# Kernel tuning notes

Hardware: AMD Instinct MI355X
Metric: run time of the kernel (lower is better)

The kernel has to match this reference:

```python
import jax, jax.numpy as jnp
import numpy as np

B, C, T = 32, 64, 4096
K = 256  # truncated memory length (kwargs['k'])


def setup_inputs() -> dict:
    key = jax.random.key(0)
    k1, k2 = jax.random.split(key)
    x = jax.random.normal(k1, (B, C, T), dtype=jnp.float32)
    epsilon = jax.random.normal(k2, (), dtype=jnp.float32)
    loc = jnp.asarray(0.5, dtype=jnp.float32)    # alpha_loc parameter
    scale = jnp.asarray(0.1, dtype=jnp.float32)  # alpha_scale parameter (pre-softplus)
    return {"x": x, "loc": loc, "scale": scale, "epsilon": epsilon, "k": K}


def _gl_coeffs(alpha, k, dtype):
    # Grunwald-Letnikov weights: w_0 = 1, w_j = w_{j-1} * (j - 1 - alpha) / j
    j = jnp.arange(k, dtype=dtype)
    factors = jnp.where(j == 0, jnp.asarray(1.0, dtype),
                        (j - 1.0 - alpha) / jnp.maximum(j, 1.0))
    return jnp.cumprod(factors)  # [k]


def reference(x, loc, scale, epsilon, k):
    # reparameterized fractional order (Normal prior): alpha = loc + softplus(scale) * eps
    alpha = loc + jax.nn.softplus(scale) * epsilon
    w = _gl_coeffs(alpha, k, x.dtype)  # [k]
    b, c, t = x.shape
    # truncated GL fractional derivative = causal depthwise conv with k taps:
    # out[n] = sum_{j=0}^{k-1} w_j * x[n-j]
    lhs = x.reshape(b * c, 1, t)                 # [N, 1, T]
    rhs = w[::-1].reshape(1, 1, k)               # [O=1, I=1, K] (flip for correlation)
    out = jax.lax.conv_general_dilated(lhs, rhs, window_strides=(1,),
                                       padding=[(k - 1, 0)])
    return out.reshape(b, c, t)
```

## Files before the change

kernel.cpp:

```cpp
#include <hip/hip_runtime.h>
#include <hip/hip_bf16.h>
#include <hip/hip_fp16.h>

#define TLEN 4096
#define KTAPS 256
#define NT 18
#define WCH 48

typedef __attribute__((ext_vector_type(8))) _Float16 f16x8;
typedef __attribute__((ext_vector_type(4))) unsigned int uint4v;
typedef __attribute__((ext_vector_type(16))) float f32x16;

static __device__ __forceinline__ unsigned int pkf16(float a, float b) {
    return __builtin_bit_cast(unsigned int, __builtin_amdgcn_cvt_pkrtz(a, b));
}

__global__ void __launch_bounds__(512, 4)
frac_conv_fused3(const float* __restrict__ x,
                 const float* __restrict__ loc,
                 const float* __restrict__ scale,
                 const float* __restrict__ eps,
                 float* __restrict__ out) {
    __shared__ unsigned int wrevp[320];
    __shared__ __align__(16) unsigned short Bf[WCH * 64 * 8];

    const int tid  = threadIdx.x;
    const int wave = tid >> 6;
    const int lane = tid & 63;
    const int l5   = lane >> 5;
    const int ln   = lane & 31;

    int rt, sg;
    {
        const int bid = blockIdx.x;
        if (gridDim.x == 512) {
            const int xcd = bid & 7;
            const int j   = bid >> 3;
            rt = xcd * 8 + (j & 7);
            sg = j >> 3;
        } else {
            rt = bid >> 3;
            sg = bid & 7;
        }
    }
    const int bn0 = sg * 512;

    const int r  = tid >> 4;
    const int cg = tid & 15;
    const float* __restrict__ xrow = x + (size_t)(rt * 32 + r) * TLEN;
    float4 v[12];
    #pragma unroll
    for (int jj = 0; jj < 12; ++jj) {
        const int w0 = cg * 4 + jj * 64;
        const int tg = bn0 - 256 + w0;
        v[jj] = (tg >= 0) ? *(const float4*)(xrow + tg) : make_float4(0.f, 0.f, 0.f, 0.f);
    }

    if (wave == 0) {
        const float alpha = loc[0] + log1pf(expf(scale[0])) * eps[0];
        const int j0 = 4 * lane;
        const float f0 = (j0 == 0) ? 1.0f : (((float)j0 - 1.0f - alpha) / (float)j0);
        const float f1 = (((float)j0 + 0.0f - alpha) / (float)(j0 + 1));
        const float f2 = (((float)j0 + 1.0f - alpha) / (float)(j0 + 2));
        const float f3 = (((float)j0 + 2.0f - alpha) / (float)(j0 + 3));
        const float p0 = f0, p1 = p0 * f1, p2 = p1 * f2, p3 = p2 * f3;
        float g = p3;
        #pragma unroll
        for (int dlt = 1; dlt < 64; dlt <<= 1) {
            const float t = __shfl_up(g, dlt, 64);
            if (lane >= dlt) g *= t;
        }
        float Sprev = __shfl_up(g, 1, 64);
        if (lane == 0) Sprev = 1.0f;
        const float q0 = Sprev * p0, q1 = Sprev * p1, q2 = Sprev * p2, q3 = g;
        const float wm1 = (lane == 0) ? 0.0f : Sprev;
        uint4v pk;
        pk[0] = pkf16(q3, q2);
        pk[1] = pkf16(q2, q1);
        pk[2] = pkf16(q1, q0);
        pk[3] = pkf16(q0, wm1);
        *(uint4v*)(wrevp + 284 - 4 * lane) = pk;
        if (lane == 63) wrevp[31] = pkf16(0.0f, q3);
        if (lane < 31)  wrevp[lane] = 0u;
        if (lane < 32)  wrevp[288 + lane] = 0u;
    }

    {
        uint2* Bf2 = (uint2*)Bf;
        #pragma unroll
        for (int jj = 0; jj < 12; ++jj) {
            const int w0 = cg * 4 + jj * 64;
            const int c  = w0 >> 4;
            const int h8 = (w0 >> 3) & 1;
            const int e0 = w0 & 7;
            const int uoff = (c * 64 + r + 32 * h8) * 8 + e0;
            Bf2[uoff >> 2] = make_uint2(pkf16(v[jj].x, v[jj].y),
                                        pkf16(v[jj].z, v[jj].w));
        }
    }
    __syncthreads();

    const int n0  = bn0 + wave * 64;
    const int lcb = wave * 4;
    const f16x8* Bv = (const f16x8*)Bf;
    const int o0 = 31 - ln + 8 * l5;

    auto LOADA = [&](int d) -> f16x8 {
        const int o = o0 + 16 * d;
        uint4v u;
        u[0] = wrevp[o];
        u[1] = wrevp[o + 2];
        u[2] = wrevp[o + 4];
        u[3] = wrevp[o + 6];
        return __builtin_bit_cast(f16x8, u);
    };

    f16x8 Afr[NT];
    f16x8 Bfr[NT + 2];
    Bfr[0] = Bv[(lcb + 0) * 64 + lane];
    Bfr[1] = Bv[(lcb + 1) * 64 + lane];
    Bfr[2] = Bv[(lcb + 2) * 64 + lane];
    Bfr[3] = Bv[(lcb + 3) * 64 + lane];
    Afr[0] = LOADA(0);
    Afr[1] = LOADA(1);

    f32x16 acc0 = {0.f, 0.f, 0.f, 0.f, 0.f, 0.f, 0.f, 0.f,
                   0.f, 0.f, 0.f, 0.f, 0.f, 0.f, 0.f, 0.f};
    f32x16 acc1 = acc0;

    #pragma unroll
    for (int d = 0; d < NT; ++d) {
        if (d + 4 < NT + 2) Bfr[d + 4] = Bv[(lcb + d + 4) * 64 + lane];
        if (d + 2 < NT)     Afr[d + 2] = LOADA(d + 2);
        acc0 = __builtin_amdgcn_mfma_f32_32x32x16_f16(Afr[d], Bfr[d],     acc0, 0, 0, 0);
        acc1 = __builtin_amdgcn_mfma_f32_32x32x16_f16(Afr[d], Bfr[d + 2], acc1, 0, 0, 0);
    }

    float* __restrict__ orow = out + (size_t)(rt * 32 + ln) * TLEN;
    #pragma unroll
    for (int g = 0; g < 4; ++g) {
        *(float4*)(orow + n0 + 8 * g + 4 * l5) =
            make_float4(acc0[4 * g + 0], acc0[4 * g + 1], acc0[4 * g + 2], acc0[4 * g + 3]);
        *(float4*)(orow + n0 + 32 + 8 * g + 4 * l5) =
            make_float4(acc1[4 * g + 0], acc1[4 * g + 1], acc1[4 * g + 2], acc1[4 * g + 3]);
    }
}

__global__ void gl_coeff_kernel(const float* __restrict__ loc,
                                const float* __restrict__ scale,
                                const float* __restrict__ eps,
                                float* __restrict__ w_out) {
    __shared__ float s[KTAPS];
    const int j = threadIdx.x;
    const float alpha = loc[0] + log1pf(expf(scale[0])) * eps[0];
    float f = (j == 0) ? 1.0f : (((float)j - 1.0f - alpha) / (float)j);
    s[j] = f;
    __syncthreads();
    #pragma unroll
    for (int st = 1; st < KTAPS; st <<= 1) {
        float v = s[j];
        float p = (j >= st) ? s[j - st] : 1.0f;
        __syncthreads();
        s[j] = v * p;
        __syncthreads();
    }
    w_out[j] = s[j];
}

__global__ void __launch_bounds__(256)
frac_conv_kernel(const float* __restrict__ x,
                 const float* __restrict__ w,
                 float* __restrict__ out) {
    __shared__ __align__(16) float xs[KTAPS + TLEN];
    __shared__ __align__(16) float wl[KTAPS];
    const int row = blockIdx.x;
    const int tid = threadIdx.x;
    const float* __restrict__ xr = x + (size_t)row * TLEN;
    float* __restrict__ orow = out + (size_t)row * TLEN;
    if (tid < 64) ((float4*)xs)[tid] = make_float4(0.f, 0.f, 0.f, 0.f);
    float4* xs4w = (float4*)(xs + KTAPS);
    const float4* xr4 = (const float4*)xr;
    #pragma unroll
    for (int k = 0; k < 4; ++k) xs4w[tid + k * 256] = xr4[tid + k * 256];
    if (tid < 64) ((float4*)wl)[tid] = ((const float4*)w)[tid];
    __syncthreads();
    const float4* __restrict__ xsv = (const float4*)xs;
    float4 acc[4]; float4 lo[4], hi[4]; int n0[4];
    #pragma unroll
    for (int g = 0; g < 4; ++g) {
        n0[g] = (tid << 2) + (g << 10);
        acc[g] = make_float4(0.f, 0.f, 0.f, 0.f);
        const int c = n0[g] >> 2;
        hi[g] = xsv[64 + c];
        lo[g] = xsv[63 + c];
    }
    #pragma unroll 4
    for (int j = 0; j < KTAPS - 4; j += 4) {
        const float4 w4 = *(const float4*)(wl + j);
        #pragma unroll
        for (int g = 0; g < 4; ++g) {
            acc[g].x += w4.x*hi[g].x + w4.y*lo[g].w + w4.z*lo[g].z + w4.w*lo[g].y;
            acc[g].y += w4.x*hi[g].y + w4.y*hi[g].x + w4.z*lo[g].w + w4.w*lo[g].z;
            acc[g].z += w4.x*hi[g].z + w4.y*hi[g].y + w4.z*hi[g].x + w4.w*lo[g].w;
            acc[g].w += w4.x*hi[g].w + w4.y*hi[g].z + w4.z*hi[g].y + w4.w*hi[g].x;
            hi[g] = lo[g];
            lo[g] = xsv[64 + ((n0[g] - j - 8) >> 2)];
        }
    }
    {
        const float4 w4 = *(const float4*)(wl + (KTAPS - 4));
        #pragma unroll
        for (int g = 0; g < 4; ++g) {
            acc[g].x += w4.x*hi[g].x + w4.y*lo[g].w + w4.z*lo[g].z + w4.w*lo[g].y;
            acc[g].y += w4.x*hi[g].y + w4.y*hi[g].x + w4.z*lo[g].w + w4.w*lo[g].z;
            acc[g].z += w4.x*hi[g].z + w4.y*hi[g].y + w4.z*hi[g].x + w4.w*lo[g].w;
            acc[g].w += w4.x*hi[g].w + w4.y*hi[g].z + w4.z*hi[g].y + w4.w*hi[g].x;
        }
    }
    #pragma unroll
    for (int g = 0; g < 4; ++g) *(float4*)(orow + n0[g]) = acc[g];
}

extern "C" void kernel_launch(void* const* d_in, const int* in_sizes, int n_in,
                              void* d_out, int out_size, void* d_ws, size_t ws_size,
                              hipStream_t stream) {
    const float* x     = (const float*)d_in[0];
    const float* loc   = (const float*)d_in[1];
    const float* scale = (const float*)d_in[2];
    const float* eps   = (const float*)d_in[3];
    float* out = (float*)d_out;
    const int rows = in_sizes[0] / TLEN;

    if ((rows % 32) == 0) {
        frac_conv_fused3<<<(rows / 32) * 8, 512, 0, stream>>>(x, loc, scale, eps, out);
    } else {
        float* w = (float*)d_ws;
        gl_coeff_kernel<<<1, 256, 0, stream>>>(loc, scale, eps, w);
        frac_conv_kernel<<<rows, 256, 0, stream>>>(x, w, out);
    }
}
```

Measured before the change: 18.90 us.

## Pipeline conv over chunked time with a shared-memory ring buffer per block

Each block now covers 1024 output samples in four 256-sample chunks instead of 512 samples in one pass. A 4-slot LDS ring holds the f16 input tiles, and the next chunk's global loads are issued before the current chunk's MFMAs run. This is meant to hide global load latency and cut the redundant 256-sample halo reloads. The cost is half as many blocks (256 instead of 512), lower occupancy (launch bounds 2), and a barrier per chunk, which can serialise the work.

```diff
diff --git a/kernel.cpp b/kernel.cpp
--- a/kernel.cpp
+++ b/kernel.cpp
@@ -5,7 +5,9 @@
 #define TLEN 4096
 #define KTAPS 256
 #define NT 18
-#define WCH 48
+#define CHUNK 256
+#define NCHK 4
+#define RING 4
 
 typedef __attribute__((ext_vector_type(8))) _Float16 f16x8;
 typedef __attribute__((ext_vector_type(4))) unsigned int uint4v;
@@ -15,14 +17,14 @@
     return __builtin_bit_cast(unsigned int, __builtin_amdgcn_cvt_pkrtz(a, b));
 }
 
-__global__ void __launch_bounds__(512, 4)
-frac_conv_fused3(const float* __restrict__ x,
-                 const float* __restrict__ loc,
-                 const float* __restrict__ scale,
-                 const float* __restrict__ eps,
-                 float* __restrict__ out) {
+__global__ void __launch_bounds__(512, 2)
+frac_conv_pipe(const float* __restrict__ x,
+               const float* __restrict__ loc,
+               const float* __restrict__ scale,
+               const float* __restrict__ eps,
+               float* __restrict__ out) {
     __shared__ unsigned int wrevp[320];
-    __shared__ __align__(16) unsigned short Bf[WCH * 64 * 8];
+    __shared__ __align__(16) unsigned short Bf[RING * 16 * 64 * 8];
 
     const int tid  = threadIdx.x;
     const int wave = tid >> 6;
@@ -31,30 +33,47 @@
     const int ln   = lane & 31;
 
     int rt, sg;
-    {
-        const int bid = blockIdx.x;
-        if (gridDim.x == 512) {
-            const int xcd = bid & 7;
-            const int j   = bid >> 3;
-            rt = xcd * 8 + (j & 7);
-            sg = j >> 3;
-        } else {
-            rt = bid >> 3;
-            sg = bid & 7;
-        }
-    }
-    const int bn0 = sg * 512;
+    if (gridDim.x == 256) {
+        const int xcd = blockIdx.x & 7;
+        const int k   = blockIdx.x >> 3;
+        rt = xcd * 8 + (k >> 2);
+        sg = k & 3;
+    } else {
+        rt = blockIdx.x >> 2;
+        sg = blockIdx.x & 3;
+    }
+    const int S0 = sg * (CHUNK * NCHK);
 
     const int r  = tid >> 4;
     const int cg = tid & 15;
     const float* __restrict__ xrow = x + (size_t)(rt * 32 + r) * TLEN;
-    float4 v[12];
-    #pragma unroll
-    for (int jj = 0; jj < 12; ++jj) {
-        const int w0 = cg * 4 + jj * 64;
-        const int tg = bn0 - 256 + w0;
-        v[jj] = (tg >= 0) ? *(const float4*)(xrow + tg) : make_float4(0.f, 0.f, 0.f, 0.f);
-    }
+
+    auto ISSUE = [&](int c, float4* v) {
+        #pragma unroll
+        for (int q = 0; q < 4; ++q) {
+            const int tg = S0 + c * CHUNK + cg * 4 + q * 64;
+            v[q] = (tg >= 0) ? *(const float4*)(xrow + tg)
+                             : make_float4(0.f, 0.f, 0.f, 0.f);
+        }
+    };
+    auto WRITE = [&](int c, const float4* v) {
+        const int slot = (c + 1) & (RING - 1);
+        uint2* Bf2 = (uint2*)Bf;
+        #pragma unroll
+        for (int q = 0; q < 4; ++q) {
+            const int w0 = cg * 4 + q * 64;
+            const int kc = w0 >> 4;
+            const int h8 = (w0 >> 3) & 1;
+            const int e0 = w0 & 7;
+            const int uoff = ((slot * 16 + kc) * 64 + r + 32 * h8) * 8 + e0;
+            Bf2[uoff >> 2] = make_uint2(pkf16(v[q].x, v[q].y),
+                                        pkf16(v[q].z, v[q].w));
+        }
+    };
+
+    float4 v0[4], v1[4];
+    ISSUE(-1, v0);
+    ISSUE(0, v1);
 
     if (wave == 0) {
         const float alpha = loc[0] + log1pf(expf(scale[0])) * eps[0];
@@ -85,25 +104,13 @@
         if (lane < 32)  wrevp[288 + lane] = 0u;
     }
 
-    {
-        uint2* Bf2 = (uint2*)Bf;
-        #pragma unroll
-        for (int jj = 0; jj < 12; ++jj) {
-            const int w0 = cg * 4 + jj * 64;
-            const int c  = w0 >> 4;
-            const int h8 = (w0 >> 3) & 1;
-            const int e0 = w0 & 7;
-            const int uoff = (c * 64 + r + 32 * h8) * 8 + e0;
-            Bf2[uoff >> 2] = make_uint2(pkf16(v[jj].x, v[jj].y),
-                                        pkf16(v[jj].z, v[jj].w));
-        }
-    }
+    WRITE(-1, v0);
+    WRITE(0, v1);
     __syncthreads();
 
-    const int n0  = bn0 + wave * 64;
-    const int lcb = wave * 4;
     const f16x8* Bv = (const f16x8*)Bf;
     const int o0 = 31 - ln + 8 * l5;
+    float* __restrict__ orow = out + (size_t)(rt * 32 + ln) * TLEN;
 
     auto LOADA = [&](int d) -> f16x8 {
         const int o = o0 + 16 * d;
@@ -115,34 +122,40 @@
         return __builtin_bit_cast(f16x8, u);
     };
 
-    f16x8 Afr[NT];
-    f16x8 Bfr[NT + 2];
-    Bfr[0] = Bv[(lcb + 0) * 64 + lane];
-    Bfr[1] = Bv[(lcb + 1) * 64 + lane];
-    Bfr[2] = Bv[(lcb + 2) * 64 + lane];
-    Bfr[3] = Bv[(lcb + 3) * 64 + lane];
-    Afr[0] = LOADA(0);
-    Afr[1] = LOADA(1);
-
-    f32x16 acc0 = {0.f, 0.f, 0.f, 0.f, 0.f, 0.f, 0.f, 0.f,
-                   0.f, 0.f, 0.f, 0.f, 0.f, 0.f, 0.f, 0.f};
-    f32x16 acc1 = acc0;
-
-    #pragma unroll
-    for (int d = 0; d < NT; ++d) {
-        if (d + 4 < NT + 2) Bfr[d + 4] = Bv[(lcb + d + 4) * 64 + lane];
-        if (d + 2 < NT)     Afr[d + 2] = LOADA(d + 2);
-        acc0 = __builtin_amdgcn_mfma_f32_32x32x16_f16(Afr[d], Bfr[d],     acc0, 0, 0, 0);
-        acc1 = __builtin_amdgcn_mfma_f32_32x32x16_f16(Afr[d], Bfr[d + 2], acc1, 0, 0, 0);
-    }
-
-    float* __restrict__ orow = out + (size_t)(rt * 32 + ln) * TLEN;
-    #pragma unroll
-    for (int g = 0; g < 4; ++g) {
-        *(float4*)(orow + n0 + 8 * g + 4 * l5) =
-            make_float4(acc0[4 * g + 0], acc0[4 * g + 1], acc0[4 * g + 2], acc0[4 * g + 3]);
-        *(float4*)(orow + n0 + 32 + 8 * g + 4 * l5) =
-            make_float4(acc1[4 * g + 0], acc1[4 * g + 1], acc1[4 * g + 2], acc1[4 * g + 3]);
+    #pragma unroll
+    for (int c = 0; c < NCHK; ++c) {
+        if (c + 1 < NCHK) ISSUE(c + 1, v0);
+
+        const int kc0 = 16 * c + 2 * wave;
+        auto LDB = [&](int d) -> f16x8 {
+            return Bv[((kc0 + d) & 63) * 64 + lane];
+        };
+
+        f16x8 Afr[NT];
+        f16x8 Bfr[NT];
+        Bfr[0] = LDB(0); Bfr[1] = LDB(1); Bfr[2] = LDB(2); Bfr[3] = LDB(3);
+        Afr[0] = LOADA(0); Afr[1] = LOADA(1);
+
+        f32x16 acc = {0.f, 0.f, 0.f, 0.f, 0.f, 0.f, 0.f, 0.f,
+                      0.f, 0.f, 0.f, 0.f, 0.f, 0.f, 0.f, 0.f};
+        #pragma unroll
+        for (int d = 0; d < NT; ++d) {
+            if (d + 4 < NT) Bfr[d + 4] = LDB(d + 4);
+            if (d + 2 < NT) Afr[d + 2] = LOADA(d + 2);
+            acc = __builtin_amdgcn_mfma_f32_32x32x16_f16(Afr[d], Bfr[d], acc, 0, 0, 0);
+        }
+
+        const int n0 = S0 + c * CHUNK + wave * 32;
+        #pragma unroll
+        for (int g = 0; g < 4; ++g) {
+            *(float4*)(orow + n0 + 8 * g + 4 * l5) =
+                make_float4(acc[4 * g + 0], acc[4 * g + 1], acc[4 * g + 2], acc[4 * g + 3]);
+        }
+
+        if (c + 1 < NCHK) {
+            WRITE(c + 1, v0);
+            __syncthreads();
+        }
     }
 }
 
@@ -232,7 +245,7 @@
     const int rows = in_sizes[0] / TLEN;
 
     if ((rows % 32) == 0) {
-        frac_conv_fused3<<<(rows / 32) * 8, 512, 0, stream>>>(x, loc, scale, eps, out);
+        frac_conv_pipe<<<(rows / 32) * 4, 512, 0, stream>>>(x, loc, scale, eps, out);
     } else {
         float* w = (float*)d_ws;
         gl_coeff_kernel<<<1, 256, 0, stream>>>(loc, scale, eps, w);
```

New measurement: 20.07 us. 1.06x slower.
